# Performance work log

Measured on AMD Instinct MI355X. Metric: run time of the kernel, lower is better.

Reference implementation:

```python
import jax, jax.numpy as jnp
import numpy as np

NUM_HEADS = 16
TEMPERATURE = 1.0


def setup_inputs() -> dict:
    key = jax.random.key(0)
    ks = jax.random.split(key, 6)
    B, H = 2048, 2048
    return {
        "hidden_states": jax.random.normal(ks[0], (B, H), dtype=jnp.float32),
        "attention_mask": jnp.ones((B,), dtype=bool),
        "Wq": jax.random.normal(ks[1], (H, H), dtype=jnp.float32) * 0.02,
        "Wk": jax.random.normal(ks[2], (H, H), dtype=jnp.float32) * 0.02,
        "Wv": jax.random.normal(ks[3], (H, H), dtype=jnp.float32) * 0.02,
        "Wo": jax.random.normal(ks[4], (H, H), dtype=jnp.float32) * 0.02,
        "scale_param": jnp.full((1,), -3.0, dtype=jnp.float32),
    }


def reference(hidden_states, attention_mask, Wq, Wk, Wv, Wo, scale_param):
    B, H = hidden_states.shape
    nh = NUM_HEADS
    hd = H // nh
    # projections (torch Linear: x @ W.T), reshape to [heads, batch, head_dim]
    q = (hidden_states @ Wq.T).reshape(B, nh, hd).transpose(1, 0, 2)
    k = (hidden_states @ Wk.T).reshape(B, nh, hd).transpose(1, 0, 2)
    v = (hidden_states @ Wv.T).reshape(B, nh, hd).transpose(1, 0, 2)
    # cross-batch scores [heads, B, B]
    scores = jnp.einsum('hqd,hkd->hqk', q, k) / (hd ** 0.5 * TEMPERATURE)
    neg_inf = jnp.float32(-jnp.inf)
    eye = jnp.eye(B, dtype=bool)  # exclude self-attention (diagonal)
    scores = jnp.where(eye[None, :, :], neg_inf, scores)
    scores = jnp.where(attention_mask[None, None, :], scores, neg_inf)
    attn = jax.nn.softmax(scores, axis=-1)
    attn = jnp.nan_to_num(attn, nan=0.0)  # rows fully masked -> 0 (dropout=0 is identity)
    ctx = jnp.einsum('hqk,hkd->hqd', attn, v)  # [heads, B, head_dim]
    ctx = ctx.transpose(1, 0, 2).reshape(B, H)
    cross = ctx @ Wo.T
    scale = jax.nn.sigmoid(scale_param[0])
    return hidden_states + scale * cross
```

## Files before the change

kernel.cpp:

```cpp
#include <hip/hip_runtime.h>

typedef __bf16 bf16;
typedef __attribute__((ext_vector_type(8))) __bf16 bf16x8;
typedef __attribute__((ext_vector_type(4))) float f32x4;
typedef __attribute__((ext_vector_type(4))) short s16x4;

#define HDIM 2048

__device__ __forceinline__ void glds16(const void* g, void* l) {
  __builtin_amdgcn_global_load_lds((const __attribute__((address_space(1))) void*)g,
                                   (__attribute__((address_space(3))) void*)l,
                                   16, 0, 0);
}

#define MFMA16(a, b, c) __builtin_amdgcn_mfma_f32_16x16x32_bf16(a, b, c, 0, 0, 0)

__global__ __launch_bounds__(256) void cvt5(
    const float* __restrict__ s0, const float* __restrict__ s1,
    const float* __restrict__ s2, const float* __restrict__ s3,
    const float* __restrict__ s4,
    bf16* __restrict__ d0, bf16* __restrict__ d1, bf16* __restrict__ d2,
    bf16* __restrict__ d3, bf16* __restrict__ d4) {
  const float* s; bf16* d;
  switch (blockIdx.y) {
    case 0: s = s0; d = d0; break;
    case 1: s = s1; d = d1; break;
    case 2: s = s2; d = d2; break;
    case 3: s = s3; d = d3; break;
    default: s = s4; d = d4; break;
  }
  const size_t base = (size_t)blockIdx.x * 4096 + (threadIdx.x << 2);
  for (int i = 0; i < 4; i++) {
    const float4 v = *(const float4*)(s + base + i * 1024);
    union { bf16 h[4]; s16x4 s4v; } u;
    u.h[0] = (bf16)v.x; u.h[1] = (bf16)v.y; u.h[2] = (bf16)v.z; u.h[3] = (bf16)v.w;
    *(s16x4*)(d + base + i * 1024) = u.s4v;
  }
}

__device__ __forceinline__ void gemm128_core(const bf16* __restrict__ A,
                                             const bf16* __restrict__ B,
                                             int rowBase, int colBase,
                                             f32x4 acc[4][4],
                                             bf16* ldsA, bf16* ldsB) {
  const int t = threadIdx.x;
  const int w = t >> 6, l = t & 63;
  const int wr = (w >> 1) << 6, wc = (w & 1) << 6;
  const int lr = l & 15, lq = l >> 4;

  for (int mi = 0; mi < 4; mi++)
    for (int ni = 0; ni < 4; ni++)
      for (int r = 0; r < 4; r++) acc[mi][ni][r] = 0.f;

  const int sRow = (w << 4) + (l >> 2);
  const int sCol = (l & 3) << 3;
  const bf16* gA = A + (size_t)(rowBase + sRow) * HDIM + sCol;
  const bf16* gB = B + (size_t)(colBase + sRow) * HDIM + sCol;
  bf16* lA = ldsA + (w << 9);
  bf16* lB = ldsB + (w << 9);

  for (int k0 = 0; k0 < HDIM; k0 += 32) {
    glds16(gA, lA);
    glds16(gA + (size_t)64 * HDIM, lA + 2048);
    glds16(gB, lB);
    glds16(gB + (size_t)64 * HDIM, lB + 2048);
    gA += 32; gB += 32;
    __syncthreads();

    bf16x8 af[4], bfr[4];
    for (int mi = 0; mi < 4; mi++)
      af[mi] = *(const bf16x8*)&ldsA[(wr + mi * 16 + lr) * 32 + lq * 8];
    for (int ni = 0; ni < 4; ni++)
      bfr[ni] = *(const bf16x8*)&ldsB[(wc + ni * 16 + lr) * 32 + lq * 8];
    for (int mi = 0; mi < 4; mi++)
      for (int ni = 0; ni < 4; ni++)
        acc[mi][ni] = MFMA16(af[mi], bfr[ni], acc[mi][ni]);
    __syncthreads();
  }
}

__global__ __launch_bounds__(256) void qkv_gemm(
    const bf16* __restrict__ hs, const bf16* __restrict__ Wq,
    const bf16* __restrict__ Wk, const bf16* __restrict__ Wv,
    bf16* __restrict__ qb, bf16* __restrict__ Kf, bf16* __restrict__ Vf) {
  __shared__ bf16 ldsA[128 * 32];
  __shared__ bf16 ldsB[128 * 32];
  const int z = blockIdx.z;
  const bf16* W = (z == 0) ? Wq : (z == 1) ? Wk : Wv;
  const int rowBase = blockIdx.y << 7, colBase = blockIdx.x << 7;
  f32x4 acc[4][4];
  gemm128_core(hs, W, rowBase, colBase, acc, ldsA, ldsB);

  const int t = threadIdx.x;
  const int w = t >> 6, l = t & 63;
  const int wr = (w >> 1) << 6, wc = (w & 1) << 6;
  const int lr = l & 15, lq = l >> 4;

  if (z == 0) {
    for (int mi = 0; mi < 4; mi++)
      for (int ni = 0; ni < 4; ni++) {
        const int col = colBase + wc + ni * 16 + lr;
        const int row0 = rowBase + wr + mi * 16 + lq * 4;
        for (int r = 0; r < 4; r++)
          qb[(size_t)(row0 + r) * HDIM + col] = (bf16)acc[mi][ni][r];
      }
  } else if (z == 1) {
    for (int mi = 0; mi < 4; mi++)
      for (int ni = 0; ni < 4; ni++) {
        const int dim = colBase + wc + ni * 16 + lr;
        const int hh = dim >> 7, ks = (dim >> 5) & 3, kh = (dim >> 3) & 3, j = dim & 7;
        const int row0 = rowBase + wr + mi * 16 + lq * 4;
        for (int r = 0; r < 4; r++) {
          const int key = row0 + r;
          const int kbk = key >> 7, kni = (key >> 4) & 7, kl = key & 15;
          Kf[(((size_t)hh * 16 + kbk) * 32 + kni * 4 + ks) * 512 +
             (kh * 16 + kl) * 8 + j] = (bf16)acc[mi][ni][r];
        }
      }
  } else {
    for (int mi = 0; mi < 4; mi++)
      for (int ni = 0; ni < 4; ni++) {
        const int dim = colBase + wc + ni * 16 + lr;
        const int hh = dim >> 7, vni = (dim >> 4) & 7, ll = dim & 15;
        const int row0 = rowBase + wr + mi * 16 + lq * 4;
        const int kbk = row0 >> 7, ks = (row0 >> 5) & 3, lh = (row0 >> 3) & 3;
        const int j0 = row0 & 7;
        union { bf16 h4[4]; s16x4 v; } u;
        for (int r = 0; r < 4; r++) u.h4[r] = (bf16)acc[mi][ni][r];
        *(s16x4*)&Vf[(((size_t)hh * 16 + kbk) * 32 + vni * 4 + ks) * 512 +
                     (lh * 16 + ll) * 8 + j0] = u.v;
      }
  }
}

__global__ __launch_bounds__(256, 2) void attn_kernel(
    const bf16* __restrict__ qb, const bf16* __restrict__ Kf,
    const bf16* __restrict__ Vf, const unsigned char* __restrict__ amask,
    bf16* __restrict__ ctx) {
  __shared__ bf16 Kl[32 * 512];
  __shared__ bf16 Vl[32 * 512];
  __shared__ bf16 Pl[4 * 16 * 128];

  const int qt = blockIdx.x, h = blockIdx.y;
  const int t = threadIdx.x, w = t >> 6, l = t & 63;
  const int lr = l & 15, lq = l >> 4;
  bf16* Pw = Pl + (w << 11);

  bf16x8 aq[4];
  for (int ks = 0; ks < 4; ks++)
    aq[ks] = *(const bf16x8*)&qb[(size_t)(qt * 64 + w * 16 + lr) * HDIM +
                                 h * 128 + ks * 32 + lq * 8];

  f32x4 o[8];
  for (int ni = 0; ni < 8; ni++)
    for (int r = 0; r < 4; r++) o[ni][r] = 0.f;
  float lsum[4] = {0.f, 0.f, 0.f, 0.f};
  int qrow[4];
  for (int r = 0; r < 4; r++) qrow[r] = qt * 64 + w * 16 + lq * 4 + r;

  const float c = 0.08838834764831845f * 1.4426950408889634f;

  for (int kbk = 0; kbk < 16; kbk++) {
    const size_t tileOff = ((size_t)h * 16 + kbk) * 32 * 512;

    for (int i = 0; i < 8; i++) {
      const int frag = i * 4 + w;
      glds16(Kf + tileOff + frag * 512 + l * 8, Kl + frag * 512);
    }
    bf16x8 vtmp[8];
    for (int i = 0; i < 8; i++) {
      const int frag = i * 4 + w;
      vtmp[i] = *(const bf16x8*)&Vf[tileOff + frag * 512 + l * 8];
    }
    for (int i = 0; i < 8; i++) {
      const int frag = i * 4 + w;
      *(bf16x8*)&Vl[frag * 512 + l * 8] = vtmp[i];
    }
    __syncthreads();

    f32x4 s[8];
    for (int ni = 0; ni < 8; ni++)
      for (int r = 0; r < 4; r++) s[ni][r] = 0.f;
    for (int ks = 0; ks < 4; ks++) {
      bf16x8 bk[8];
      for (int ni = 0; ni < 8; ni++)
        bk[ni] = *(const bf16x8*)&Kl[(ni * 4 + ks) * 512 + l * 8];
      for (int ni = 0; ni < 8; ni++) s[ni] = MFMA16(aq[ks], bk[ni], s[ni]);
    }

    float mk[8];
    for (int ni = 0; ni < 8; ni++)
      mk[ni] = amask[kbk * 128 + ni * 16 + lr] ? 1.f : 0.f;
    const bool diagBlk = (kbk == (qt >> 1));
    for (int ni = 0; ni < 8; ni++) {
      const int col = kbk * 128 + ni * 16 + lr;
      for (int r = 0; r < 4; r++) {
        float p = __builtin_exp2f(s[ni][r] * c) * mk[ni];
        if (diagBlk && col == qrow[r]) p = 0.f;
        s[ni][r] = p;
        lsum[r] += p;
      }
    }

    for (int ni = 0; ni < 8; ni++)
      for (int r = 0; r < 4; r++) {
        const int row = lq * 4 + r;
        Pw[row * 128 + (((ni * 2 + (lr >> 3)) ^ row) << 3) + (lr & 7)] = (bf16)s[ni][r];
      }

    for (int ks = 0; ks < 4; ks++) {
      bf16x8 bv[8];
      for (int ni = 0; ni < 8; ni++)
        bv[ni] = *(const bf16x8*)&Vl[(ni * 4 + ks) * 512 + l * 8];
      const bf16x8 ap = *(const bf16x8*)&Pw[lr * 128 + (((ks * 4 + lq) ^ lr) << 3)];
      for (int ni = 0; ni < 8; ni++) o[ni] = MFMA16(ap, bv[ni], o[ni]);
    }
    __syncthreads();
  }

  for (int r = 0; r < 4; r++)
    for (int off = 1; off < 16; off <<= 1)
      lsum[r] += __shfl_xor(lsum[r], off);

  for (int ni = 0; ni < 8; ni++)
    for (int r = 0; r < 4; r++) {
      const int row = qrow[r];
      const int col = h * 128 + ni * 16 + lr;
      const float li = lsum[r];
      ctx[(size_t)row * HDIM + col] = (bf16)((li > 0.f) ? o[ni][r] / li : 0.f);
    }
}

__global__ __launch_bounds__(256) void out_gemm(
    const bf16* __restrict__ ctx, const bf16* __restrict__ Wo,
    const float* __restrict__ hs, const float* __restrict__ scale_p,
    float* __restrict__ outp) {
  __shared__ bf16 ldsA[128 * 32];
  __shared__ bf16 ldsB[64 * 32];
  const int rowBase = blockIdx.y << 7, colBase = blockIdx.x << 6;
  const int t = threadIdx.x;
  const int w = t >> 6, l = t & 63;
  const int wr = (w >> 1) << 6, wc = (w & 1) << 5;
  const int lr = l & 15, lq = l >> 4;

  f32x4 acc[4][2];
  for (int mi = 0; mi < 4; mi++)
    for (int ni = 0; ni < 2; ni++)
      for (int r = 0; r < 4; r++) acc[mi][ni][r] = 0.f;

  const int sRow = (w << 4) + (l >> 2);
  const int sCol = (l & 3) << 3;
  const bf16* gA = ctx + (size_t)(rowBase + sRow) * HDIM + sCol;
  const bf16* gB = Wo + (size_t)(colBase + sRow) * HDIM + sCol;
  bf16* lA = ldsA + (w << 9);
  bf16* lB = ldsB + (w << 9);

  for (int k0 = 0; k0 < HDIM; k0 += 32) {
    glds16(gA, lA);
    glds16(gA + (size_t)64 * HDIM, lA + 2048);
    glds16(gB, lB);
    gA += 32; gB += 32;
    __syncthreads();

    bf16x8 af[4], bfr[2];
    for (int mi = 0; mi < 4; mi++)
      af[mi] = *(const bf16x8*)&ldsA[(wr + mi * 16 + lr) * 32 + lq * 8];
    for (int ni = 0; ni < 2; ni++)
      bfr[ni] = *(const bf16x8*)&ldsB[(wc + ni * 16 + lr) * 32 + lq * 8];
    for (int mi = 0; mi < 4; mi++)
      for (int ni = 0; ni < 2; ni++)
        acc[mi][ni] = MFMA16(af[mi], bfr[ni], acc[mi][ni]);
    __syncthreads();
  }

  const float sig = 1.0f / (1.0f + __expf(-scale_p[0]));
  for (int mi = 0; mi < 4; mi++)
    for (int ni = 0; ni < 2; ni++) {
      const int col = colBase + wc + ni * 16 + lr;
      const int row0 = rowBase + wr + mi * 16 + lq * 4;
      for (int r = 0; r < 4; r++) {
        const size_t idx = (size_t)(row0 + r) * HDIM + col;
        outp[idx] = hs[idx] + sig * acc[mi][ni][r];
      }
    }
}

extern "C" void kernel_launch(void* const* d_in, const int* in_sizes, int n_in,
                              void* d_out, int out_size, void* d_ws, size_t ws_size,
                              hipStream_t stream) {
  const float* hs = (const float*)d_in[0];
  const unsigned char* amask = (const unsigned char*)d_in[1];
  const float* Wq = (const float*)d_in[2];
  const float* Wk = (const float*)d_in[3];
  const float* Wv = (const float*)d_in[4];
  const float* Wo = (const float*)d_in[5];
  const float* scale_p = (const float*)d_in[6];
  float* outp = (float*)d_out;

  const size_t N = (size_t)HDIM * HDIM;
  bf16* qb   = (bf16*)d_ws;
  bf16* Kf   = qb + N;
  bf16* Vf   = Kf + N;
  bf16* ctx  = Vf + N;
  bf16* hs16 = ctx + N;
  bf16* Wq16 = hs16 + N;
  bf16* Wk16 = Wq16 + N;
  bf16* Wv16 = Wk16 + N;
  bf16* Wo16 = Wv16 + N;

  cvt5<<<dim3(1024, 5), 256, 0, stream>>>(hs, Wq, Wk, Wv, Wo,
                                          hs16, Wq16, Wk16, Wv16, Wo16);
  qkv_gemm<<<dim3(16, 16, 3), 256, 0, stream>>>(hs16, Wq16, Wk16, Wv16, qb, Kf, Vf);
  attn_kernel<<<dim3(32, 16), 256, 0, stream>>>(qb, Kf, Vf, amask, ctx);
  out_gemm<<<dim3(32, 16), 256, 0, stream>>>(ctx, Wo16, hs, scale_p, outp);
}
```

Baseline: 279.7 us.

## Split attention waves into 2x2 row/key groups and reduce partial outputs

Each wave now handles 32 query rows over half of each 128-key tile instead of 16 rows over the full tile. K fragments are reused across two query row sets and V fragments across two P sets, which halves LDS reads per MFMA. Partial outputs and row sums from the two key-group waves are combined through shared memory at the end. The cost is more accumulator registers (o doubles to 16 f32x4) plus an extra barrier and LDS reduction pass.

Measured after the change: 289.5 us. 1.03x slower.

```diff
diff --git a/kernel.cpp b/kernel.cpp
--- a/kernel.cpp
+++ b/kernel.cpp
@@ -139,24 +139,29 @@
     bf16* __restrict__ ctx) {
   __shared__ bf16 Kl[32 * 512];
   __shared__ bf16 Vl[32 * 512];
-  __shared__ bf16 Pl[4 * 16 * 128];
+  __shared__ bf16 Pl[4 * 32 * 64];
 
   const int qt = blockIdx.x, h = blockIdx.y;
   const int t = threadIdx.x, w = t >> 6, l = t & 63;
   const int lr = l & 15, lq = l >> 4;
+  const int rg = w >> 1;
+  const int kg = w & 1;
   bf16* Pw = Pl + (w << 11);
 
-  bf16x8 aq[4];
-  for (int ks = 0; ks < 4; ks++)
-    aq[ks] = *(const bf16x8*)&qb[(size_t)(qt * 64 + w * 16 + lr) * HDIM +
-                                 h * 128 + ks * 32 + lq * 8];
-
-  f32x4 o[8];
-  for (int ni = 0; ni < 8; ni++)
-    for (int r = 0; r < 4; r++) o[ni][r] = 0.f;
-  float lsum[4] = {0.f, 0.f, 0.f, 0.f};
-  int qrow[4];
-  for (int r = 0; r < 4; r++) qrow[r] = qt * 64 + w * 16 + lq * 4 + r;
+  bf16x8 aq[2][4];
+  for (int set = 0; set < 2; set++)
+    for (int ks = 0; ks < 4; ks++)
+      aq[set][ks] = *(const bf16x8*)&qb[(size_t)(qt * 64 + rg * 32 + set * 16 + lr) * HDIM +
+                                        h * 128 + ks * 32 + lq * 8];
+
+  f32x4 o[2][8];
+  for (int set = 0; set < 2; set++)
+    for (int ni = 0; ni < 8; ni++)
+      for (int r = 0; r < 4; r++) o[set][ni][r] = 0.f;
+  float lsum[2][4];
+  for (int set = 0; set < 2; set++)
+    for (int r = 0; r < 4; r++) lsum[set][r] = 0.f;
+  const int qrowBase = qt * 64 + rg * 32 + lq * 4;
 
   const float c = 0.08838834764831845f * 1.4426950408889634f;
 
@@ -178,57 +183,82 @@
     }
     __syncthreads();
 
-    f32x4 s[8];
-    for (int ni = 0; ni < 8; ni++)
-      for (int r = 0; r < 4; r++) s[ni][r] = 0.f;
+    f32x4 s[2][4];
+    for (int set = 0; set < 2; set++)
+      for (int ni = 0; ni < 4; ni++)
+        for (int r = 0; r < 4; r++) s[set][ni][r] = 0.f;
     for (int ks = 0; ks < 4; ks++) {
-      bf16x8 bk[8];
-      for (int ni = 0; ni < 8; ni++)
-        bk[ni] = *(const bf16x8*)&Kl[(ni * 4 + ks) * 512 + l * 8];
-      for (int ni = 0; ni < 8; ni++) s[ni] = MFMA16(aq[ks], bk[ni], s[ni]);
-    }
-
-    float mk[8];
-    for (int ni = 0; ni < 8; ni++)
-      mk[ni] = amask[kbk * 128 + ni * 16 + lr] ? 1.f : 0.f;
+      bf16x8 bk[4];
+      for (int ni = 0; ni < 4; ni++)
+        bk[ni] = *(const bf16x8*)&Kl[((kg * 4 + ni) * 4 + ks) * 512 + l * 8];
+      for (int set = 0; set < 2; set++)
+        for (int ni = 0; ni < 4; ni++)
+          s[set][ni] = MFMA16(aq[set][ks], bk[ni], s[set][ni]);
+    }
+
+    float mk[4];
+    for (int ni = 0; ni < 4; ni++)
+      mk[ni] = amask[kbk * 128 + kg * 64 + ni * 16 + lr] ? 1.f : 0.f;
     const bool diagBlk = (kbk == (qt >> 1));
-    for (int ni = 0; ni < 8; ni++) {
-      const int col = kbk * 128 + ni * 16 + lr;
-      for (int r = 0; r < 4; r++) {
-        float p = __builtin_exp2f(s[ni][r] * c) * mk[ni];
-        if (diagBlk && col == qrow[r]) p = 0.f;
-        s[ni][r] = p;
-        lsum[r] += p;
-      }
-    }
-
-    for (int ni = 0; ni < 8; ni++)
-      for (int r = 0; r < 4; r++) {
-        const int row = lq * 4 + r;
-        Pw[row * 128 + (((ni * 2 + (lr >> 3)) ^ row) << 3) + (lr & 7)] = (bf16)s[ni][r];
-      }
-
-    for (int ks = 0; ks < 4; ks++) {
+    for (int set = 0; set < 2; set++)
+      for (int ni = 0; ni < 4; ni++) {
+        const int col = kbk * 128 + kg * 64 + ni * 16 + lr;
+        for (int r = 0; r < 4; r++) {
+          float p = __builtin_exp2f(s[set][ni][r] * c) * mk[ni];
+          if (diagBlk && col == qrowBase + set * 16 + r) p = 0.f;
+          lsum[set][r] += p;
+          const int row = set * 16 + lq * 4 + r;
+          const int swz = (row ^ (row >> 2)) & 7;
+          Pw[row * 64 + (((ni * 2 + (lr >> 3)) ^ swz) << 3) + (lr & 7)] = (bf16)p;
+        }
+      }
+
+    for (int ksp = 0; ksp < 2; ksp++) {
       bf16x8 bv[8];
       for (int ni = 0; ni < 8; ni++)
-        bv[ni] = *(const bf16x8*)&Vl[(ni * 4 + ks) * 512 + l * 8];
-      const bf16x8 ap = *(const bf16x8*)&Pw[lr * 128 + (((ks * 4 + lq) ^ lr) << 3)];
-      for (int ni = 0; ni < 8; ni++) o[ni] = MFMA16(ap, bv[ni], o[ni]);
-    }
-    __syncthreads();
-  }
-
-  for (int r = 0; r < 4; r++)
-    for (int off = 1; off < 16; off <<= 1)
-      lsum[r] += __shfl_xor(lsum[r], off);
-
-  for (int ni = 0; ni < 8; ni++)
-    for (int r = 0; r < 4; r++) {
-      const int row = qrow[r];
-      const int col = h * 128 + ni * 16 + lr;
-      const float li = lsum[r];
-      ctx[(size_t)row * HDIM + col] = (bf16)((li > 0.f) ? o[ni][r] / li : 0.f);
-    }
+        bv[ni] = *(const bf16x8*)&Vl[(ni * 4 + kg * 2 + ksp) * 512 + l * 8];
+      for (int set = 0; set < 2; set++) {
+        const int row = set * 16 + lr;
+        const int swz = (row ^ (row >> 2)) & 7;
+        const bf16x8 ap = *(const bf16x8*)&Pw[row * 64 + (((ksp * 4 + lq) ^ swz) << 3)];
+        for (int ni = 0; ni < 8; ni++) o[set][ni] = MFMA16(ap, bv[ni], o[set][ni]);
+      }
+    }
+    __syncthreads();
+  }
+
+  for (int set = 0; set < 2; set++)
+    for (int r = 0; r < 4; r++)
+      for (int off = 1; off < 16; off <<= 1)
+        lsum[set][r] += __shfl_xor(lsum[set][r], off);
+
+  float* obuf = rg ? (float*)Vl : (float*)Kl;
+  float* lbuf = (float*)Pl;
+  if (kg == 1) {
+    for (int set = 0; set < 2; set++)
+      for (int ni = 0; ni < 8; ni++)
+        for (int r = 0; r < 4; r++)
+          obuf[(set * 16 + lq * 4 + r) * 128 + ni * 16 + lr] = o[set][ni][r];
+    if (lr == 0)
+      for (int set = 0; set < 2; set++)
+        for (int r = 0; r < 4; r++)
+          lbuf[rg * 32 + set * 16 + lq * 4 + r] = lsum[set][r];
+  }
+  __syncthreads();
+  if (kg == 0) {
+    for (int set = 0; set < 2; set++)
+      for (int r = 0; r < 4; r++)
+        lsum[set][r] += lbuf[rg * 32 + set * 16 + lq * 4 + r];
+    for (int set = 0; set < 2; set++)
+      for (int ni = 0; ni < 8; ni++)
+        for (int r = 0; r < 4; r++) {
+          const float ov = o[set][ni][r] + obuf[(set * 16 + lq * 4 + r) * 128 + ni * 16 + lr];
+          const int row = qrowBase + set * 16 + r;
+          const int col = h * 128 + ni * 16 + lr;
+          const float li = lsum[set][r];
+          ctx[(size_t)row * HDIM + col] = (bf16)((li > 0.f) ? ov / li : 0.f);
+        }
+  }
 }
 
 __global__ __launch_bounds__(256) void out_gemm(
```
